# Kernel tuning notes

Hardware: AMD Instinct MI355X
Metric: run time of the kernel (lower is better)

Reference implementation:

```python
import jax, jax.numpy as jnp
import numpy as np

B, S, E, H, D = 4, 2048, 1024, 16, 64

def setup_inputs() -> dict:
    key = jax.random.key(0)
    ks = jax.random.split(key, 9)
    sc = 0.02
    return {
        "x":  jax.random.normal(ks[0], (B, S, E), jnp.float32),
        "Wq": jax.random.normal(ks[1], (H, E, D), jnp.float32) * sc,
        "bq": jax.random.normal(ks[2], (H, D), jnp.float32) * sc,
        "Wk": jax.random.normal(ks[3], (H, E, D), jnp.float32) * sc,
        "bk": jax.random.normal(ks[4], (H, D), jnp.float32) * sc,
        "Wv": jax.random.normal(ks[5], (H, E, D), jnp.float32) * sc,
        "bv": jax.random.normal(ks[6], (H, D), jnp.float32) * sc,
        "Wp": jax.random.normal(ks[7], (H * D, E), jnp.float32) * sc,
        "bp": jax.random.normal(ks[8], (E,), jnp.float32) * sc,
    }

def reference(x, Wq, bq, Wk, bk, Wv, bv, Wp, bp):
    # Per-head projections (stacked): [B,S,E] x [H,E,D] -> [B,H,S,D]
    q = jnp.einsum('bse,hed->bhsd', x, Wq) + bq[None, :, None, :]
    k = jnp.einsum('bse,hed->bhsd', x, Wk) + bk[None, :, None, :]
    v = jnp.einsum('bse,hed->bhsd', x, Wv) + bv[None, :, None, :]
    # Scaled scores with causal mask: [B,H,S,S]
    scores = jnp.einsum('bhqd,bhkd->bhqk', q, k) / jnp.sqrt(jnp.float32(D))
    causal = jnp.tril(jnp.ones((S, S), dtype=bool))
    scores = jnp.where(causal[None, None], scores, -jnp.inf)
    attn = jax.nn.softmax(scores, axis=-1)
    out = jnp.einsum('bhqk,bhkd->bhqd', attn, v)          # [B,H,S,D]
    out = out.transpose(0, 2, 1, 3).reshape(B, S, H * D)  # concat heads
    return out @ Wp + bp                                   # [B,S,E]
```

## Files before the change

kernel.cpp:

```cpp
#include <hip/hip_runtime.h>
#include <hip/hip_bf16.h>

#define B_ 4
#define S_ 2048
#define E_ 1024
#define H_ 16
#define D_ 64
#define QSCALE 0.18033688011112042f

typedef __attribute__((ext_vector_type(8))) short bf16x8;
typedef __attribute__((ext_vector_type(4))) float f32x4;
typedef __attribute__((ext_vector_type(16))) float f32x16;

__device__ __forceinline__ f32x4 mfma16(bf16x8 a, bf16x8 b, f32x4 c) {
    return __builtin_amdgcn_mfma_f32_16x16x32_bf16(a, b, c, 0, 0, 0);
}
__device__ __forceinline__ f32x16 mfma32(bf16x8 a, bf16x8 b, f32x16 c) {
    return __builtin_amdgcn_mfma_f32_32x32x16_bf16(a, b, c, 0, 0, 0);
}
__device__ __forceinline__ short f2bs(float f) {
    __hip_bfloat16 h = __float2bfloat16(f);
    return *reinterpret_cast<short*>(&h);
}

#define XSLAB 1032
#define WSLAB 1544

__global__ __launch_bounds__(256) void conv_wqkv(
    const float* __restrict__ Wq, const float* __restrict__ Wk,
    const float* __restrict__ Wv, short* __restrict__ WT)
{
    const int mat = blockIdx.x >> 4;
    const int kt  = blockIdx.x & 15;
    const int which = mat >> 4, h = mat & 15;
    const float* src = (which == 0 ? Wq : which == 1 ? Wk : Wv) + (size_t)h * E_ * D_;
    __shared__ float T[64][65];
    const int tid = threadIdx.x;
    const int k0 = kt * 64;
    #pragma unroll
    for (int it = 0; it < 4; ++it) {
        int lin = tid + it * 256;
        int kr = lin >> 4, dc = (lin & 15) * 4;
        const float4 v = *(const float4*)&src[(size_t)(k0 + kr) * D_ + dc];
        T[kr][dc] = v.x; T[kr][dc + 1] = v.y; T[kr][dc + 2] = v.z; T[kr][dc + 3] = v.w;
    }
    __syncthreads();
    #pragma unroll
    for (int it = 0; it < 4; ++it) {
        int lin = tid + it * 256;
        int dr = lin >> 4, kc = (lin & 15) * 4;
        ushort4 o;
        o.x = (unsigned short)f2bs(T[kc][dr]);
        o.y = (unsigned short)f2bs(T[kc + 1][dr]);
        o.z = (unsigned short)f2bs(T[kc + 2][dr]);
        o.w = (unsigned short)f2bs(T[kc + 3][dr]);
        *(ushort4*)&WT[((size_t)mat * 64 + dr) * E_ + k0 + kc] = o;
    }
}

__global__ __launch_bounds__(256) void conv_wp(
    const float* __restrict__ Wp, short* __restrict__ WpT)
{
    const int ktile = blockIdx.x & 15, ntile = blockIdx.x >> 4;
    const int k0 = ktile * 64, n0 = ntile * 64;
    __shared__ float T[64][65];
    const int tid = threadIdx.x;
    #pragma unroll
    for (int it = 0; it < 4; ++it) {
        int lin = tid + it * 256;
        int kr = lin >> 4, nc = (lin & 15) * 4;
        const float4 v = *(const float4*)&Wp[(size_t)(k0 + kr) * E_ + n0 + nc];
        T[kr][nc] = v.x; T[kr][nc + 1] = v.y; T[kr][nc + 2] = v.z; T[kr][nc + 3] = v.w;
    }
    __syncthreads();
    #pragma unroll
    for (int it = 0; it < 4; ++it) {
        int lin = tid + it * 256;
        int nr = lin >> 4, kc = (lin & 15) * 4;
        ushort4 o;
        o.x = (unsigned short)f2bs(T[kc][nr]);
        o.y = (unsigned short)f2bs(T[kc + 1][nr]);
        o.z = (unsigned short)f2bs(T[kc + 2][nr]);
        o.w = (unsigned short)f2bs(T[kc + 3][nr]);
        *(ushort4*)&WpT[(size_t)(n0 + nr) * E_ + k0 + kc] = o;
    }
}

__global__ __launch_bounds__(256, 2) void qkv_fused(
    const float* __restrict__ x, const short* __restrict__ WT,
    const float* __restrict__ bq, const float* __restrict__ bk,
    const float* __restrict__ bv,
    short* __restrict__ Qw, short* __restrict__ Kw, short* __restrict__ VTw)
{
    const int h = blockIdx.y;
    const int m0 = blockIdx.x * 128;
    __shared__ short SM[8 * XSLAB + 8 * WSLAB];
    short* Xs = SM;
    short* Ws = SM + 8 * XSLAB;

    const int tid = threadIdx.x;
    const int lane = tid & 63, w = tid >> 6;
    const int wm = w & 1, wn = w >> 1;
    const int l31 = lane & 31, hi = lane >> 5;
    const int cc = tid & 7, r8 = tid >> 3;

    f32x16 acc[2][3];
    #pragma unroll
    for (int mf = 0; mf < 2; ++mf)
        #pragma unroll
        for (int nf = 0; nf < 3; ++nf)
            #pragma unroll
            for (int i = 0; i < 16; ++i) acc[mf][nf][i] = 0.f;

    float4 xr[4][2];
    bf16x8 wr[6];

    #pragma unroll
    for (int it = 0; it < 4; ++it) {
        const float* p = &x[(size_t)(m0 + it * 32 + r8) * E_ + cc * 8];
        xr[it][0] = *(const float4*)p;
        xr[it][1] = *(const float4*)(p + 4);
    }
    #pragma unroll
    for (int it = 0; it < 6; ++it) {
        int rg = ((it >> 1) * 16 + h) * 64 + (it & 1) * 32 + r8;
        wr[it] = *(const bf16x8*)&WT[(size_t)rg * E_ + cc * 8];
    }

    for (int k0 = 0; k0 < E_; k0 += 64) {
        #pragma unroll
        for (int it = 0; it < 4; ++it) {
            bf16x8 pk;
            pk[0] = f2bs(xr[it][0].x); pk[1] = f2bs(xr[it][0].y);
            pk[2] = f2bs(xr[it][0].z); pk[3] = f2bs(xr[it][0].w);
            pk[4] = f2bs(xr[it][1].x); pk[5] = f2bs(xr[it][1].y);
            pk[6] = f2bs(xr[it][1].z); pk[7] = f2bs(xr[it][1].w);
            *(bf16x8*)&Xs[cc * XSLAB + (it * 32 + r8) * 8] = pk;
        }
        #pragma unroll
        for (int it = 0; it < 6; ++it)
            *(bf16x8*)&Ws[cc * WSLAB + (it * 32 + r8) * 8] = wr[it];
        __syncthreads();
        if (k0 + 64 < E_) {
            #pragma unroll
            for (int it = 0; it < 4; ++it) {
                const float* p = &x[(size_t)(m0 + it * 32 + r8) * E_ + k0 + 64 + cc * 8];
                xr[it][0] = *(const float4*)p;
                xr[it][1] = *(const float4*)(p + 4);
            }
            #pragma unroll
            for (int it = 0; it < 6; ++it) {
                int rg = ((it >> 1) * 16 + h) * 64 + (it & 1) * 32 + r8;
                wr[it] = *(const bf16x8*)&WT[(size_t)rg * E_ + k0 + 64 + cc * 8];
            }
        }
        #pragma unroll
        for (int ks = 0; ks < 4; ++ks) {
            const int ccr = ks * 2 + hi;
            bf16x8 a[2], b[3];
            #pragma unroll
            for (int mf = 0; mf < 2; ++mf)
                a[mf] = *(const bf16x8*)&Xs[ccr * XSLAB + (wm * 64 + mf * 32 + l31) * 8];
            #pragma unroll
            for (int nf = 0; nf < 3; ++nf)
                b[nf] = *(const bf16x8*)&Ws[ccr * WSLAB + (wn * 96 + nf * 32 + l31) * 8];
            #pragma unroll
            for (int mf = 0; mf < 2; ++mf)
                #pragma unroll
                for (int nf = 0; nf < 3; ++nf)
                    acc[mf][nf] = mfma32(a[mf], b[nf], acc[mf][nf]);
        }
        __syncthreads();
    }

    const int bb = m0 >> 11;
    const int s0 = m0 & (S_ - 1);
    const size_t qkbase = ((size_t)bb * H_ + h) * S_;
    short* Vr = SM;
    #pragma unroll
    for (int mf = 0; mf < 2; ++mf)
        #pragma unroll
        for (int nf = 0; nf < 3; ++nf) {
            const int ng = wn * 96 + nf * 32;
            const int mat = ng >> 6;
            const int d = (ng & 63) + l31;
            const int sl0 = wm * 64 + mf * 32 + 4 * hi;
            if (mat == 0) {
                const float bb_ = bq[h * D_ + d];
                #pragma unroll
                for (int rg = 0; rg < 16; ++rg) {
                    int s = s0 + sl0 + (rg & 3) + 8 * (rg >> 2);
                    Qw[(qkbase + s) * D_ + d] = f2bs((acc[mf][nf][rg] + bb_) * QSCALE);
                }
            } else if (mat == 1) {
                const float bb_ = bk[h * D_ + d];
                #pragma unroll
                for (int rg = 0; rg < 16; ++rg) {
                    int s = s0 + sl0 + (rg & 3) + 8 * (rg >> 2);
                    Kw[(qkbase + s) * D_ + d] = f2bs(acc[mf][nf][rg] + bb_);
                }
            } else {
                const float bb_ = bv[h * D_ + d];
                #pragma unroll
                for (int rg = 0; rg < 16; ++rg) {
                    int sl = sl0 + (rg & 3) + 8 * (rg >> 2);
                    Vr[d * 136 + sl] = f2bs(acc[mf][nf][rg] + bb_);
                }
            }
        }
    __syncthreads();
    const size_t vbase = ((size_t)bb * H_ + h) * (size_t)D_ * S_;
    const int sc = tid & 15, dr = tid >> 4;
    #pragma unroll
    for (int it = 0; it < 4; ++it) {
        int d = it * 16 + dr;
        *(bf16x8*)&VTw[vbase + (size_t)d * S_ + s0 + sc * 8] =
            *(const bf16x8*)&Vr[d * 136 + sc * 8];
    }
}

__global__ __launch_bounds__(256, 2) void attn(
    const short* __restrict__ Qw, const short* __restrict__ Kw,
    const short* __restrict__ VTw, short* __restrict__ Ow)
{
    const int jj = blockIdx.x;
    const int bh = blockIdx.y;
    const int b = bh >> 4, h = bh & 15;
    const size_t kbase = ((size_t)b * H_ + h) * (size_t)S_ * D_;
    const size_t vbase = ((size_t)b * H_ + h) * (size_t)D_ * S_;

    __shared__ short Qs[128 * 72];
    __shared__ short Ks[2][64 * 72];
    __shared__ short Vt[2][64 * 72];

    const int tid = threadIdx.x;
    const int lane = tid & 63, w = tid >> 6;
    const int l15 = lane & 15, qd = lane >> 4;

    const int r0s = tid >> 3;
    const int c0s = (tid & 7) * 8;
    const int r1s = r0s + 32;

    #pragma unroll
    for (int phase = 0; phase < 2; ++phase) {
        const int qt = phase ? jj : (15 - jj);

        #pragma unroll
        for (int it = 0; it < 4; ++it) {
            int row = w * 32 + it * 8 + (lane >> 3);
            int cb = (lane & 7) * 8;
            *(bf16x8*)&Qs[row * 72 + cb] =
                *(const bf16x8*)&Qw[kbase + (size_t)(qt * 128 + row) * D_ + cb];
        }
        asm volatile("s_waitcnt lgkmcnt(0)" ::: "memory");
        bf16x8 qf[2][2];
        #pragma unroll
        for (int mi = 0; mi < 2; ++mi)
            #pragma unroll
            for (int t = 0; t < 2; ++t)
                qf[mi][t] = *(const bf16x8*)&Qs[(w * 32 + mi * 16 + l15) * 72 + t * 32 + qd * 8];

        f32x4 zero = {0.f, 0.f, 0.f, 0.f};
        f32x4 oacc[2][4];
        float lrow[2][4];
        #pragma unroll
        for (int mi = 0; mi < 2; ++mi) {
            #pragma unroll
            for (int c = 0; c < 4; ++c) oacc[mi][c] = zero;
            #pragma unroll
            for (int r = 0; r < 4; ++r) lrow[mi][r] = 0.f;
        }

        const int nkt = (qt + 1) * 2;
        bf16x8 kr0, kr1, vr0, vr1;
        kr0 = *(const bf16x8*)&Kw[kbase + (size_t)r0s * D_ + c0s];
        kr1 = *(const bf16x8*)&Kw[kbase + (size_t)r1s * D_ + c0s];
        vr0 = *(const bf16x8*)&VTw[vbase + (size_t)r0s * S_ + c0s];
        vr1 = *(const bf16x8*)&VTw[vbase + (size_t)r1s * S_ + c0s];
        *(bf16x8*)&Ks[0][r0s * 72 + c0s] = kr0;
        *(bf16x8*)&Ks[0][r1s * 72 + c0s] = kr1;
        *(bf16x8*)&Vt[0][r0s * 72 + c0s] = vr0;
        *(bf16x8*)&Vt[0][r1s * 72 + c0s] = vr1;
        __syncthreads();

        int p = 0;
        for (int kt = 0; kt < nkt; ++kt) {
            const bool pre = (kt + 1 < nkt);
            if (pre) {
                kr0 = *(const bf16x8*)&Kw[kbase + (size_t)((kt + 1) * 64 + r0s) * D_ + c0s];
                kr1 = *(const bf16x8*)&Kw[kbase + (size_t)((kt + 1) * 64 + r1s) * D_ + c0s];
                vr0 = *(const bf16x8*)&VTw[vbase + (size_t)r0s * S_ + (kt + 1) * 64 + c0s];
                vr1 = *(const bf16x8*)&VTw[vbase + (size_t)r1s * S_ + (kt + 1) * 64 + c0s];
            }
            f32x4 sc[2][4];
            #pragma unroll
            for (int mi = 0; mi < 2; ++mi)
                #pragma unroll
                for (int c = 0; c < 4; ++c) sc[mi][c] = zero;
            #pragma unroll
            for (int t = 0; t < 2; ++t)
                #pragma unroll
                for (int c = 0; c < 4; ++c) {
                    bf16x8 bk = *(const bf16x8*)&Ks[p][(c * 16 + l15) * 72 + t * 32 + qd * 8];
                    sc[0][c] = mfma16(qf[0][t], bk, sc[0][c]);
                    sc[1][c] = mfma16(qf[1][t], bk, sc[1][c]);
                }
            #pragma unroll
            for (int mi = 0; mi < 2; ++mi) {
                const int fr = qt * 128 + w * 32 + mi * 16;
                if (kt * 64 + 63 > fr) {
                    #pragma unroll
                    for (int c = 0; c < 4; ++c) {
                        int col = kt * 64 + c * 16 + l15;
                        #pragma unroll
                        for (int r = 0; r < 4; ++r)
                            if (col > fr + qd * 4 + r) sc[mi][c][r] = -1e30f;
                    }
                }
                #pragma unroll
                for (int c = 0; c < 4; ++c)
                    #pragma unroll
                    for (int r = 0; r < 4; ++r) {
                        float pv = __builtin_amdgcn_exp2f(sc[mi][c][r]);
                        lrow[mi][r] += pv;
                        Qs[(w * 32 + mi * 16 + qd * 4 + r) * 72 + c * 16 + l15] = f2bs(pv);
                    }
            }
            asm volatile("s_waitcnt lgkmcnt(0)" ::: "memory");
            #pragma unroll
            for (int t = 0; t < 2; ++t) {
                bf16x8 ap0 = *(const bf16x8*)&Qs[(w * 32 + l15) * 72 + t * 32 + qd * 8];
                bf16x8 ap1 = *(const bf16x8*)&Qs[(w * 32 + 16 + l15) * 72 + t * 32 + qd * 8];
                #pragma unroll
                for (int c = 0; c < 4; ++c) {
                    bf16x8 bv = *(const bf16x8*)&Vt[p][(c * 16 + l15) * 72 + t * 32 + qd * 8];
                    oacc[0][c] = mfma16(ap0, bv, oacc[0][c]);
                    oacc[1][c] = mfma16(ap1, bv, oacc[1][c]);
                }
            }
            if (pre) {
                *(bf16x8*)&Ks[1 - p][r0s * 72 + c0s] = kr0;
                *(bf16x8*)&Ks[1 - p][r1s * 72 + c0s] = kr1;
                *(bf16x8*)&Vt[1 - p][r0s * 72 + c0s] = vr0;
                *(bf16x8*)&Vt[1 - p][r1s * 72 + c0s] = vr1;
            }
            __syncthreads();
            p ^= 1;
        }

        #pragma unroll
        for (int mi = 0; mi < 2; ++mi) {
            float inv[4];
            #pragma unroll
            for (int r = 0; r < 4; ++r) {
                float l = lrow[mi][r];
                l += __shfl_xor(l, 1);
                l += __shfl_xor(l, 2);
                l += __shfl_xor(l, 4);
                l += __shfl_xor(l, 8);
                inv[r] = 1.f / l;
            }
            #pragma unroll
            for (int c = 0; c < 4; ++c)
                #pragma unroll
                for (int r = 0; r < 4; ++r) {
                    int s = qt * 128 + w * 32 + mi * 16 + qd * 4 + r;
                    Ow[((size_t)b * S_ + s) * (H_ * D_) + h * D_ + c * 16 + l15] =
                        f2bs(oacc[mi][c][r] * inv[r]);
                }
        }
    }
}

__global__ __launch_bounds__(256, 2) void out_proj(
    const short* __restrict__ Oin, const short* __restrict__ WpT,
    const float* __restrict__ bp, float* __restrict__ out)
{
    const int m0 = blockIdx.x * 128;
    const int n0 = blockIdx.y * 128;
    __shared__ short SM2[16 * XSLAB];
    short* As = SM2;
    short* Bs = SM2 + 8 * XSLAB;

    const int tid = threadIdx.x;
    const int lane = tid & 63, w = tid >> 6;
    const int wm = w & 1, wn = w >> 1;
    const int l31 = lane & 31, hi = lane >> 5;
    const int cc = tid & 7, r8 = tid >> 3;

    f32x16 acc[2][2];
    #pragma unroll
    for (int mf = 0; mf < 2; ++mf)
        #pragma unroll
        for (int nf = 0; nf < 2; ++nf)
            #pragma unroll
            for (int i = 0; i < 16; ++i) acc[mf][nf][i] = 0.f;

    bf16x8 ar[4], br[4];
    #pragma unroll
    for (int it = 0; it < 4; ++it) {
        ar[it] = *(const bf16x8*)&Oin[(size_t)(m0 + it * 32 + r8) * E_ + cc * 8];
        br[it] = *(const bf16x8*)&WpT[(size_t)(n0 + it * 32 + r8) * E_ + cc * 8];
    }

    for (int k0 = 0; k0 < E_; k0 += 64) {
        #pragma unroll
        for (int it = 0; it < 4; ++it) {
            *(bf16x8*)&As[cc * XSLAB + (it * 32 + r8) * 8] = ar[it];
            *(bf16x8*)&Bs[cc * XSLAB + (it * 32 + r8) * 8] = br[it];
        }
        __syncthreads();
        if (k0 + 64 < E_) {
            #pragma unroll
            for (int it = 0; it < 4; ++it) {
                ar[it] = *(const bf16x8*)&Oin[(size_t)(m0 + it * 32 + r8) * E_ + k0 + 64 + cc * 8];
                br[it] = *(const bf16x8*)&WpT[(size_t)(n0 + it * 32 + r8) * E_ + k0 + 64 + cc * 8];
            }
        }
        #pragma unroll
        for (int ks = 0; ks < 4; ++ks) {
            const int ccr = ks * 2 + hi;
            bf16x8 a[2], b[2];
            #pragma unroll
            for (int mf = 0; mf < 2; ++mf)
                a[mf] = *(const bf16x8*)&As[ccr * XSLAB + (wm * 64 + mf * 32 + l31) * 8];
            #pragma unroll
            for (int nf = 0; nf < 2; ++nf)
                b[nf] = *(const bf16x8*)&Bs[ccr * XSLAB + (wn * 64 + nf * 32 + l31) * 8];
            #pragma unroll
            for (int mf = 0; mf < 2; ++mf)
                #pragma unroll
                for (int nf = 0; nf < 2; ++nf)
                    acc[mf][nf] = mfma32(a[mf], b[nf], acc[mf][nf]);
        }
        __syncthreads();
    }
    #pragma unroll
    for (int mf = 0; mf < 2; ++mf)
        #pragma unroll
        for (int nf = 0; nf < 2; ++nf) {
            const int n = n0 + wn * 64 + nf * 32 + l31;
            const float bpv = bp[n];
            const int sl0 = wm * 64 + mf * 32 + 4 * hi;
            #pragma unroll
            for (int rg = 0; rg < 16; ++rg) {
                int m = m0 + sl0 + (rg & 3) + 8 * (rg >> 2);
                out[(size_t)m * E_ + n] = acc[mf][nf][rg] + bpv;
            }
        }
}

extern "C" void kernel_launch(void* const* d_in, const int* in_sizes, int n_in,
                              void* d_out, int out_size, void* d_ws, size_t ws_size,
                              hipStream_t stream)
{
    const float* x  = (const float*)d_in[0];
    const float* Wq = (const float*)d_in[1];
    const float* bq = (const float*)d_in[2];
    const float* Wk = (const float*)d_in[3];
    const float* bk = (const float*)d_in[4];
    const float* Wv = (const float*)d_in[5];
    const float* bv = (const float*)d_in[6];
    const float* Wp = (const float*)d_in[7];
    const float* bp = (const float*)d_in[8];
    float* out = (float*)d_out;

    const size_t nQKV = (size_t)B_ * H_ * S_ * D_;
    short* Qw   = (short*)d_ws;
    short* Kw   = Qw + nQKV;
    short* VTw  = Kw + nQKV;
    short* buf3 = VTw + nQKV;
    short* WT   = buf3;
    short* Ow   = buf3;
    short* WpT  = Qw;

    conv_wqkv<<<dim3(768), 256, 0, stream>>>(Wq, Wk, Wv, WT);
    qkv_fused<<<dim3(64, 16), 256, 0, stream>>>(x, WT, bq, bk, bv, Qw, Kw, VTw);
    attn<<<dim3(8, 64), 256, 0, stream>>>(Qw, Kw, VTw, Ow);
    conv_wp<<<dim3(256), 256, 0, stream>>>(Wp, WpT);
    out_proj<<<dim3(64, 8), 256, 0, stream>>>(Ow, WpT, bp, out);
}
```

Before: 252.3 us.

## Pre-convert x to bf16 and load GEMM A operands directly from global

Adds a separate conversion kernel that turns x into bf16 once, so the QKV projection no longer re-reads fp32 x and re-converts it for each of the 16 heads. In both the QKV and output-projection GEMMs, the A operand is now loaded straight from global memory into registers in MFMA fragment layout, skipping LDS staging and halving shared memory per block. The weight buffer moves into the output buffer to make room for the bf16 copy of x. The cost is an extra launch and a round trip of x through memory, and the A loads are no longer prefetched one tile ahead, so they depend on cache hits.

```diff
diff --git a/kernel.cpp b/kernel.cpp
--- a/kernel.cpp
+++ b/kernel.cpp
@@ -23,8 +23,20 @@
     return *reinterpret_cast<short*>(&h);
 }
 
-#define XSLAB 1032
 #define WSLAB 1544
+#define BSLAB 1032
+
+__global__ __launch_bounds__(256) void conv_x(
+    const float* __restrict__ x, short* __restrict__ xb)
+{
+    const size_t i = ((size_t)blockIdx.x * 256 + threadIdx.x) * 8;
+    const float4 v0 = *(const float4*)&x[i];
+    const float4 v1 = *(const float4*)&x[i + 4];
+    bf16x8 pk;
+    pk[0] = f2bs(v0.x); pk[1] = f2bs(v0.y); pk[2] = f2bs(v0.z); pk[3] = f2bs(v0.w);
+    pk[4] = f2bs(v1.x); pk[5] = f2bs(v1.y); pk[6] = f2bs(v1.z); pk[7] = f2bs(v1.w);
+    *(bf16x8*)&xb[i] = pk;
+}
 
 __global__ __launch_bounds__(256) void conv_wqkv(
     const float* __restrict__ Wq, const float* __restrict__ Wk,
@@ -87,16 +99,14 @@
 }
 
 __global__ __launch_bounds__(256, 2) void qkv_fused(
-    const float* __restrict__ x, const short* __restrict__ WT,
+    const short* __restrict__ xb, const short* __restrict__ WT,
     const float* __restrict__ bq, const float* __restrict__ bk,
     const float* __restrict__ bv,
     short* __restrict__ Qw, short* __restrict__ Kw, short* __restrict__ VTw)
 {
     const int h = blockIdx.y;
     const int m0 = blockIdx.x * 128;
-    __shared__ short SM[8 * XSLAB + 8 * WSLAB];
-    short* Xs = SM;
-    short* Ws = SM + 8 * XSLAB;
+    __shared__ short Ws[8 * WSLAB];
 
     const int tid = threadIdx.x;
     const int lane = tid & 63, w = tid >> 6;
@@ -112,55 +122,38 @@
             #pragma unroll
             for (int i = 0; i < 16; ++i) acc[mf][nf][i] = 0.f;
 
-    float4 xr[4][2];
     bf16x8 wr[6];
-
-    #pragma unroll
-    for (int it = 0; it < 4; ++it) {
-        const float* p = &x[(size_t)(m0 + it * 32 + r8) * E_ + cc * 8];
-        xr[it][0] = *(const float4*)p;
-        xr[it][1] = *(const float4*)(p + 4);
-    }
     #pragma unroll
     for (int it = 0; it < 6; ++it) {
         int rg = ((it >> 1) * 16 + h) * 64 + (it & 1) * 32 + r8;
         wr[it] = *(const bf16x8*)&WT[(size_t)rg * E_ + cc * 8];
     }
 
+    const short* ar0 = &xb[(size_t)(m0 + wm * 64 + l31) * E_ + hi * 8];
+    const short* ar1 = ar0 + (size_t)32 * E_;
+
     for (int k0 = 0; k0 < E_; k0 += 64) {
-        #pragma unroll
-        for (int it = 0; it < 4; ++it) {
-            bf16x8 pk;
-            pk[0] = f2bs(xr[it][0].x); pk[1] = f2bs(xr[it][0].y);
-            pk[2] = f2bs(xr[it][0].z); pk[3] = f2bs(xr[it][0].w);
-            pk[4] = f2bs(xr[it][1].x); pk[5] = f2bs(xr[it][1].y);
-            pk[6] = f2bs(xr[it][1].z); pk[7] = f2bs(xr[it][1].w);
-            *(bf16x8*)&Xs[cc * XSLAB + (it * 32 + r8) * 8] = pk;
-        }
         #pragma unroll
         for (int it = 0; it < 6; ++it)
             *(bf16x8*)&Ws[cc * WSLAB + (it * 32 + r8) * 8] = wr[it];
         __syncthreads();
         if (k0 + 64 < E_) {
             #pragma unroll
-            for (int it = 0; it < 4; ++it) {
-                const float* p = &x[(size_t)(m0 + it * 32 + r8) * E_ + k0 + 64 + cc * 8];
-                xr[it][0] = *(const float4*)p;
-                xr[it][1] = *(const float4*)(p + 4);
-            }
-            #pragma unroll
             for (int it = 0; it < 6; ++it) {
                 int rg = ((it >> 1) * 16 + h) * 64 + (it & 1) * 32 + r8;
                 wr[it] = *(const bf16x8*)&WT[(size_t)rg * E_ + k0 + 64 + cc * 8];
             }
         }
+        bf16x8 a[2][4];
+        #pragma unroll
+        for (int ks = 0; ks < 4; ++ks) {
+            a[0][ks] = *(const bf16x8*)&ar0[k0 + ks * 16];
+            a[1][ks] = *(const bf16x8*)&ar1[k0 + ks * 16];
+        }
         #pragma unroll
         for (int ks = 0; ks < 4; ++ks) {
             const int ccr = ks * 2 + hi;
-            bf16x8 a[2], b[3];
-            #pragma unroll
-            for (int mf = 0; mf < 2; ++mf)
-                a[mf] = *(const bf16x8*)&Xs[ccr * XSLAB + (wm * 64 + mf * 32 + l31) * 8];
+            bf16x8 b[3];
             #pragma unroll
             for (int nf = 0; nf < 3; ++nf)
                 b[nf] = *(const bf16x8*)&Ws[ccr * WSLAB + (wn * 96 + nf * 32 + l31) * 8];
@@ -168,7 +161,7 @@
             for (int mf = 0; mf < 2; ++mf)
                 #pragma unroll
                 for (int nf = 0; nf < 3; ++nf)
-                    acc[mf][nf] = mfma32(a[mf], b[nf], acc[mf][nf]);
+                    acc[mf][nf] = mfma32(a[mf][ks], b[nf], acc[mf][nf]);
         }
         __syncthreads();
     }
@@ -176,7 +169,7 @@
     const int bb = m0 >> 11;
     const int s0 = m0 & (S_ - 1);
     const size_t qkbase = ((size_t)bb * H_ + h) * S_;
-    short* Vr = SM;
+    short* Vr = Ws;
     #pragma unroll
     for (int mf = 0; mf < 2; ++mf)
         #pragma unroll
@@ -378,9 +371,7 @@
 {
     const int m0 = blockIdx.x * 128;
     const int n0 = blockIdx.y * 128;
-    __shared__ short SM2[16 * XSLAB];
-    short* As = SM2;
-    short* Bs = SM2 + 8 * XSLAB;
+    __shared__ short Bs[8 * BSLAB];
 
     const int tid = threadIdx.x;
     const int lane = tid & 63, w = tid >> 6;
@@ -396,42 +387,42 @@
             #pragma unroll
             for (int i = 0; i < 16; ++i) acc[mf][nf][i] = 0.f;
 
-    bf16x8 ar[4], br[4];
-    #pragma unroll
-    for (int it = 0; it < 4; ++it) {
-        ar[it] = *(const bf16x8*)&Oin[(size_t)(m0 + it * 32 + r8) * E_ + cc * 8];
+    bf16x8 br[4];
+    #pragma unroll
+    for (int it = 0; it < 4; ++it)
         br[it] = *(const bf16x8*)&WpT[(size_t)(n0 + it * 32 + r8) * E_ + cc * 8];
-    }
+
+    const short* ar0 = &Oin[(size_t)(m0 + wm * 64 + l31) * E_ + hi * 8];
+    const short* ar1 = ar0 + (size_t)32 * E_;
 
     for (int k0 = 0; k0 < E_; k0 += 64) {
         #pragma unroll
-        for (int it = 0; it < 4; ++it) {
-            *(bf16x8*)&As[cc * XSLAB + (it * 32 + r8) * 8] = ar[it];
-            *(bf16x8*)&Bs[cc * XSLAB + (it * 32 + r8) * 8] = br[it];
-        }
+        for (int it = 0; it < 4; ++it)
+            *(bf16x8*)&Bs[cc * BSLAB + (it * 32 + r8) * 8] = br[it];
         __syncthreads();
         if (k0 + 64 < E_) {
             #pragma unroll
-            for (int it = 0; it < 4; ++it) {
-                ar[it] = *(const bf16x8*)&Oin[(size_t)(m0 + it * 32 + r8) * E_ + k0 + 64 + cc * 8];
+            for (int it = 0; it < 4; ++it)
                 br[it] = *(const bf16x8*)&WpT[(size_t)(n0 + it * 32 + r8) * E_ + k0 + 64 + cc * 8];
-            }
+        }
+        bf16x8 a[2][4];
+        #pragma unroll
+        for (int ks = 0; ks < 4; ++ks) {
+            a[0][ks] = *(const bf16x8*)&ar0[k0 + ks * 16];
+            a[1][ks] = *(const bf16x8*)&ar1[k0 + ks * 16];
         }
         #pragma unroll
         for (int ks = 0; ks < 4; ++ks) {
             const int ccr = ks * 2 + hi;
-            bf16x8 a[2], b[2];
+            bf16x8 b[2];
+            #pragma unroll
+            for (int nf = 0; nf < 2; ++nf)
+                b[nf] = *(const bf16x8*)&Bs[ccr * BSLAB + (wn * 64 + nf * 32 + l31) * 8];
             #pragma unroll
             for (int mf = 0; mf < 2; ++mf)
-                a[mf] = *(const bf16x8*)&As[ccr * XSLAB + (wm * 64 + mf * 32 + l31) * 8];
-            #pragma unroll
-            for (int nf = 0; nf < 2; ++nf)
-                b[nf] = *(const bf16x8*)&Bs[ccr * XSLAB + (wn * 64 + nf * 32 + l31) * 8];
-            #pragma unroll
-            for (int mf = 0; mf < 2; ++mf)
                 #pragma unroll
                 for (int nf = 0; nf < 2; ++nf)
-                    acc[mf][nf] = mfma32(a[mf], b[nf], acc[mf][nf]);
+                    acc[mf][nf] = mfma32(a[mf][ks], b[nf], acc[mf][nf]);
         }
         __syncthreads();
     }
@@ -470,12 +461,14 @@
     short* Kw   = Qw + nQKV;
     short* VTw  = Kw + nQKV;
     short* buf3 = VTw + nQKV;
-    short* WT   = buf3;
+    short* xbuf = buf3;
     short* Ow   = buf3;
+    short* WT   = (short*)d_out;
     short* WpT  = Qw;
 
+    conv_x<<<dim3(4096), 256, 0, stream>>>(x, xbuf);
     conv_wqkv<<<dim3(768), 256, 0, stream>>>(Wq, Wk, Wv, WT);
-    qkv_fused<<<dim3(64, 16), 256, 0, stream>>>(x, WT, bq, bk, bv, Qw, Kw, VTw);
+    qkv_fused<<<dim3(64, 16), 256, 0, stream>>>(xbuf, WT, bq, bk, bv, Qw, Kw, VTw);
     attn<<<dim3(8, 64), 256, 0, stream>>>(Qw, Kw, VTw, Ow);
     conv_wp<<<dim3(256), 256, 0, stream>>>(Wp, WpT);
     out_proj<<<dim3(64, 8), 256, 0, stream>>>(Ow, WpT, bp, out);
```

Result: slower. 306.4 us (+21.5%).
